# Kernel tuning notes

Measured on AMD Instinct MI355X. Metric: run time of the kernel, lower is better.

Reference implementation:

```python
import jax, jax.numpy as jnp
import numpy as np

B, C, N, L, K, PRED = 64, 2, 1024, 24, 3, 12


def setup_inputs() -> dict:
    key = jax.random.key(0)
    ks = jax.random.split(key, 32)
    u = lambda k, shape, s: jax.random.uniform(k, shape, jnp.float32, -s, s)
    stdv_gc = 1.0 / np.sqrt(N)
    stdv_g = 1.0 / np.sqrt(N * (K + 1))
    stdv_r = 1.0 / np.sqrt(2 * N)
    inp = {
        'inputs': jax.random.normal(ks[0], (B, C, N, L), jnp.float32),
        'adj': (jax.random.uniform(ks[1], (N, N)) < 0.05).astype(jnp.float32),
        'gc_w': u(ks[2], (K, N, N), stdv_gc),
        'Wf': u(ks[3], (N, N * (K + 1)), stdv_g), 'bf': u(ks[4], (N,), stdv_g),
        'Wi': u(ks[5], (N, N * (K + 1)), stdv_g), 'bi': u(ks[6], (N,), stdv_g),
        'Wo': u(ks[7], (N, N * (K + 1)), stdv_g), 'bo': u(ks[8], (N,), stdv_g),
        'Wc': u(ks[9], (N, N * (K + 1)), stdv_g), 'bc': u(ks[10], (N,), stdv_g),
        'rWf': u(ks[11], (N, 2 * N), stdv_r), 'rbf': u(ks[12], (N,), stdv_r),
        'rWi': u(ks[13], (N, 2 * N), stdv_r), 'rbi': u(ks[14], (N,), stdv_r),
        'rWo': u(ks[15], (N, 2 * N), stdv_r), 'rbo': u(ks[16], (N,), stdv_r),
        'rWc': u(ks[17], (N, 2 * N), stdv_r), 'rbc': u(ks[18], (N,), stdv_r),
        'neighbor_w': u(ks[19], (N,), stdv_gc),
        'c': jnp.ones((1,), jnp.float32),
        'conv_w': u(ks[20], (C * PRED, C), 1.0 / np.sqrt(C)),
        'conv_b': u(ks[21], (C * PRED,), 1.0 / np.sqrt(C)),
    }
    return inp


def _build_A_list(adj, k):
    # tmp = sum(A, 0); zeros -> 1e-5; 'D_inverse' = diag(tmp) (as in original code)
    tmp = jnp.sum(adj, 0)
    tmp = jnp.where(tmp == 0, 1e-5, tmp)
    a_norm = tmp[:, None] * adj  # diag(tmp) @ A
    a_list = []
    a_tmp = jnp.eye(adj.shape[0], dtype=adj.dtype)
    for _ in range(k):
        a_tmp = jnp.minimum(a_tmp @ a_norm, 1.0)  # clamp max=1.0
        a_list.append(a_tmp)
    return a_list


def _forward(adj, inputs, gc_w, Wf, bf, Wi, bi, Wo, bo, Wc, bc,
             rWf, rbf, rWi, rbi, rWo, rbo, rWc, rbc, neighbor_w, c, conv_w, conv_b):
    b, ch, n, l = inputs.shape
    k = gc_w.shape[0]
    a_list = _build_A_list(adj, k)
    a_stack = jnp.stack(a_list)            # (K,N,N)
    eff_w = a_stack * gc_w                 # masked FilterLinear weights
    nbr = a_list[-1] @ neighbor_w          # (N,)
    Wg = jnp.concatenate([Wf, Wi, Wo, Wc], 0)      # fused gate weights (4N, (K+1)N)
    bg = jnp.concatenate([bf, bi, bo, bc], 0)
    rWg = jnp.concatenate([rWf, rWi, rWo, rWc], 0)  # (4N, 2N)
    rbg = jnp.concatenate([rbf, rbi, rbo, rbc], 0)

    def step(carry, x):  # x: (B,C,N)
        H, Cs, rH, rCs, _ = carry
        # gc = cat_k FilterLinear_k(x), each x @ (A_k*W_k)^T
        gc = jnp.einsum('bcn,kmn->bckm', x, eff_w).reshape(b, ch, k * n)
        g = jnp.concatenate([gc, H], -1) @ Wg.T + bg
        f, i, o, Ct = jnp.split(g, 4, -1)
        Cs = jax.nn.sigmoid(f) * (Cs * nbr) + jax.nn.sigmoid(i) * jnp.tanh(Ct)
        H = jax.nn.sigmoid(o) * jnp.tanh(Cs)
        rg = jnp.concatenate([x, rH], -1) @ rWg.T + rbg
        rf, ri, ro, rCt = jnp.split(rg, 4, -1)
        rCs = jax.nn.sigmoid(rf) * rCs + jax.nn.sigmoid(ri) * jnp.tanh(rCt)
        rH = jax.nn.sigmoid(ro) * jnp.tanh(rCs)
        var1 = jnp.var(x, axis=(0, 2), keepdims=True, ddof=1)   # (1,C,1), unbiased like torch
        var2 = jnp.var(gc, axis=(0, 2), keepdims=True, ddof=1)
        pred = (H * var1 * c + rH * var2) / (var1 + var2 * c)
        return (H, Cs, rH, rCs, pred), None

    z = jnp.zeros((b, ch, n), inputs.dtype)
    xs = jnp.moveaxis(inputs, -1, 0)  # (L,B,C,N)
    (H, Cs, rH, rCs, pred), _ = jax.lax.scan(step, (z, z, z, z, z), xs)
    # Conv1d(C, C*pred_len, k=1) then reshape (B,C,N,pred_len)
    out = jnp.einsum('bcn,oc->bon', pred, conv_w) + conv_b[:, None]
    return out.reshape(b, ch, n, -1)


def reference(inputs, adj, gc_w, Wf, bf, Wi, bi, Wo, bo, Wc, bc,
              rWf, rbf, rWi, rbi, rWo, rbo, rWc, rbc, neighbor_w, c, conv_w, conv_b):
    return _forward(adj, inputs, gc_w, Wf, bf, Wi, bi, Wo, bo, Wc, bc,
                    rWf, rbf, rWi, rbi, rWo, rbo, rWc, rbc, neighbor_w, c, conv_w, conv_b)
```

## Files before the change

### kernel.cpp

```cpp
#include <hip/hip_runtime.h>
#include <cmath>

#define NN 1024
#define BC 128
#define LS 24

typedef unsigned short u16;
typedef __attribute__((ext_vector_type(4))) float f32x4;
typedef __attribute__((ext_vector_type(8))) short bf16x8;

typedef __attribute__((address_space(1))) const void* as1cv;
typedef __attribute__((address_space(3))) void* as3v;

#define GLD16(gp, lp) __builtin_amdgcn_global_load_lds((as1cv)(gp), (as3v)(lp), 16, 0, 0)

__device__ __forceinline__ float sigf(float x){ return 1.0f/(1.0f+expf(-x)); }

__device__ __forceinline__ u16 f2b(float x){
  union { float f; unsigned u; } v; v.f = x;
  unsigned r = v.u + 0x7FFFu + ((v.u >> 16) & 1u);
  return (u16)(r >> 16);
}
__device__ __forceinline__ float b2f(u16 b){
  union { unsigned u; float f; } v; v.u = ((unsigned)b) << 16;
  return v.f;
}


__global__ void k_transpose(const float* __restrict__ in, u16* __restrict__ Xb){
  int idx = blockIdx.x*256 + threadIdx.x;
  const float4* p = (const float4*)(in + (size_t)idx*LS);
  float v[LS];
  #pragma unroll
  for (int q = 0; q < 6; ++q){
    float4 f = p[q];
    v[q*4]=f.x; v[q*4+1]=f.y; v[q*4+2]=f.z; v[q*4+3]=f.w;
  }
  #pragma unroll
  for (int t = 0; t < LS; ++t)
    Xb[(size_t)t*BC*NN + idx] = f2b(v[t]);
}

__global__ void k_colsum1(const float* __restrict__ adj, float* __restrict__ part){
  int b = blockIdx.x;
  for (int j = threadIdx.x; j < 1024; j += 256){
    float s = 0.f;
    for (int i = 0; i < 16; ++i) s += adj[(size_t)(b*16+i)*1024 + j];
    part[(size_t)b*1024 + j] = s;
  }
}
__global__ void k_colsum2(const float* __restrict__ part, float* __restrict__ tmp){
  int j = blockIdx.x*256 + threadIdx.x;
  float s = 0.f;
  for (int b = 0; b < 64; ++b) s += part[(size_t)b*1024 + j];
  tmp[j] = (s == 0.f) ? 1e-5f : s;
}

__global__ void k_anormT(const float* __restrict__ adj, const float* __restrict__ tmp,
                         u16* __restrict__ A1b, u16* __restrict__ anormT){
  __shared__ u16 t[64][65];
  int bi = blockIdx.y*64, bj = blockIdx.x*64;
  for (int e = threadIdx.x; e < 4096; e += 256){
    int r = e >> 6, cc = e & 63;
    float v = tmp[bi+r]*adj[(size_t)(bi+r)*1024 + bj+cc];
    A1b[(size_t)(bi+r)*1024 + bj+cc] = f2b(fminf(v, 1.f));
    t[r][cc] = f2b(v);
  }
  __syncthreads();
  for (int e = threadIdx.x; e < 4096; e += 256){
    int r = e >> 6, cc = e & 63;
    anormT[(size_t)(bj+r)*1024 + bi+cc] = t[cc][r];
  }
}

__global__ void k_nbr(const u16* __restrict__ A3b, const float* __restrict__ nw,
                      float* __restrict__ nbr){
  __shared__ float red[256];
  int row = blockIdx.x;
  float s = 0.f;
  for (int j = threadIdx.x; j < 1024; j += 256)
    s += b2f(A3b[(size_t)row*1024 + j])*nw[j];
  red[threadIdx.x] = s; __syncthreads();
  for (int st = 128; st > 0; st >>= 1){
    if (threadIdx.x < st) red[threadIdx.x] += red[threadIdx.x+st];
    __syncthreads();
  }
  if (threadIdx.x == 0) nbr[row] = red[0];
}

__global__ void k_effT(const u16* __restrict__ Ap, const float* __restrict__ gcw,
                       u16* __restrict__ effb, u16* __restrict__ effbT){
  __shared__ u16 t[64][65];
  int bi = blockIdx.y*64, bj = blockIdx.x*64;
  for (int e = threadIdx.x; e < 4096; e += 256){
    int r = e >> 6, cc = e & 63;
    size_t idx = (size_t)(bi+r)*1024 + bj+cc;
    u16 v = f2b(b2f(Ap[idx]) * gcw[idx]);
    effb[idx] = v;
    t[r][cc] = v;
  }
  __syncthreads();
  for (int e = threadIdx.x; e < 4096; e += 256){
    int r = e >> 6, cc = e & 63;
    effbT[(size_t)(bj+r)*3072 + bi+cc] = t[cc][r];
  }
}

__global__ void k_pack(const float* __restrict__ Wf, const float* __restrict__ Wi,
                       const float* __restrict__ Wo, const float* __restrict__ Wc,
                       const float* __restrict__ rWf, const float* __restrict__ rWi,
                       const float* __restrict__ rWo, const float* __restrict__ rWc,
                       u16* __restrict__ Wgxb, u16* __restrict__ WgHp,
                       u16* __restrict__ rWgxb, u16* __restrict__ rWgHp){
  int idx = blockIdx.x*256 + threadIdx.x;
  if (idx < 16777216){
    int k = idx & 4095, r = idx >> 12, seg = r >> 10, j = r & 1023;
    const float* W = seg==0?Wf: seg==1?Wi: seg==2?Wo:Wc;
    float v = W[(size_t)j*4096 + k];
    if (k < 3072) Wgxb[(size_t)r*3072 + k] = f2b(v);
    else {
      int p = (j>>2)*16 + seg*4 + (j&3);
      WgHp[(size_t)p*1024 + (k-3072)] = f2b(v);
    }
  } else {
    int i2 = idx - 16777216;
    int k = i2 & 2047, r = i2 >> 11, seg = r >> 10, j = r & 1023;
    const float* W = seg==0?rWf: seg==1?rWi: seg==2?rWo:rWc;
    float v = W[(size_t)j*2048 + k];
    if (k < 1024) rWgxb[(size_t)r*1024 + k] = f2b(v);
    else {
      int p = (j>>2)*16 + seg*4 + (j&3);
      rWgHp[(size_t)p*1024 + (k-1024)] = f2b(v);
    }
  }
}
__global__ void k_packbias(const float* __restrict__ bf_, const float* __restrict__ bi_,
                           const float* __restrict__ bo_, const float* __restrict__ bc_,
                           const float* __restrict__ rbf, const float* __restrict__ rbi,
                           const float* __restrict__ rbo, const float* __restrict__ rbc,
                           float* __restrict__ bg, float* __restrict__ rbg){
  int idx = blockIdx.x*256 + threadIdx.x;
  int seg = idx >> 10, j = idx & 1023;
  bg[idx]  = (seg==0?bf_: seg==1?bi_: seg==2?bo_:bc_)[j];
  rbg[idx] = (seg==0?rbf: seg==1?rbi: seg==2?rbo:rbc)[j];
}

__device__ __forceinline__ void stage128(const u16* __restrict__ A, const u16* __restrict__ B,
                                         int K, int k0, u16* lA, u16* lB, int w, int lane){
  const int lrow = lane >> 3;
  const int srck = ((lane & 7) ^ lrow) * 8;
  #pragma unroll
  for (int c = 0; c < 4; ++c){
    int row = w*32 + c*8;
    GLD16(A + (size_t)(row + lrow)*K + k0 + srck, &lA[row*64]);
    GLD16(B + (size_t)(row + lrow)*K + k0 + srck, &lB[row*64]);
  }
}

__device__ __forceinline__ void mfma_tile(
    const u16* __restrict__ A, const u16* __restrict__ Bw, int K,
    const float* __restrict__ bias,
    float* __restrict__ outf, u16* __restrict__ outb, int ldc)
{
  __shared__ u16 ldsA[128*64];
  __shared__ u16 ldsB[128*64];
  const int tid  = threadIdx.x;
  const int lane = tid & 63;
  const int w    = tid >> 6;
  const int wr   = (w >> 1) * 64;
  const int wc   = (w & 1) * 64;
  f32x4 acc[4][4] = {};

  for (int k0 = 0; k0 < K; k0 += 64){
    stage128(A, Bw, K, k0, ldsA, ldsB, w, lane);
    __syncthreads();
    #pragma unroll
    for (int kk = 0; kk < 2; ++kk) {
      bf16x8 af[4], bfr[4];
      #pragma unroll
      for (int mi = 0; mi < 4; ++mi) {
        int row = wr + mi*16 + (lane & 15);
        int grp = (kk*4 + (lane >> 4)) ^ (row & 7);
        af[mi] = *(const bf16x8*)&ldsA[row*64 + grp*8];
      }
      #pragma unroll
      for (int ni = 0; ni < 4; ++ni) {
        int row = wc + ni*16 + (lane & 15);
        int grp = (kk*4 + (lane >> 4)) ^ (row & 7);
        bfr[ni] = *(const bf16x8*)&ldsB[row*64 + grp*8];
      }
      #pragma unroll
      for (int mi = 0; mi < 4; ++mi)
        #pragma unroll
        for (int ni = 0; ni < 4; ++ni)
          acc[mi][ni] = __builtin_amdgcn_mfma_f32_16x16x32_bf16(af[mi], bfr[ni], acc[mi][ni], 0, 0, 0);
    }
    __syncthreads();
  }
  #pragma unroll
  for (int mi = 0; mi < 4; ++mi) {
    #pragma unroll
    for (int ni = 0; ni < 4; ++ni) {
      int col = wc + ni*16 + (lane & 15);
      #pragma unroll
      for (int q = 0; q < 4; ++q) {
        int row = wr + mi*16 + (lane >> 4)*4 + q;
        float v = acc[mi][ni][q];
        if (bias) v += bias[col];
        if (outf) outf[(size_t)row*ldc + col] = v;
        if (outb) outb[(size_t)row*ldc + col] = f2b(v);
      }
    }
  }
}

__global__ __launch_bounds__(256) void k_mfma_nt(
    const u16* __restrict__ A, const u16* __restrict__ B, int K,
    const float* __restrict__ bias, float* __restrict__ outf,
    u16* __restrict__ outb, int ldc)
{
  size_t i0 = (size_t)blockIdx.y * 128, j0 = (size_t)blockIdx.x * 128;
  mfma_tile(A + i0*K, B + j0*K, K,
            bias ? bias + j0 : nullptr,
            outf ? outf + i0*ldc + j0 : nullptr,
            outb ? outb + i0*ldc + j0 : nullptr, ldc);
}

__global__ __launch_bounds__(256) void k_mfma64(
    const u16* __restrict__ Ag, const u16* __restrict__ Bg, int K,
    int clamp1, u16* __restrict__ outb, int ldc)
{
  __shared__ u16 ldsA[64*64];
  __shared__ u16 ldsB[64*64];
  const int tid  = threadIdx.x;
  const int lane = tid & 63;
  const int w    = tid >> 6;
  const int wr   = (w >> 1) * 32;
  const int wc   = (w & 1) * 32;
  const u16* A = Ag + (size_t)blockIdx.y*64*K;
  const u16* B = Bg + (size_t)blockIdx.x*64*K;
  f32x4 acc[2][2] = {};

  const int lrow = lane >> 3;
  const int srck = ((lane & 7) ^ lrow) * 8;
  for (int k0 = 0; k0 < K; k0 += 64){
    #pragma unroll
    for (int c = 0; c < 2; ++c){
      int row = w*16 + c*8;
      GLD16(A + (size_t)(row + lrow)*K + k0 + srck, &ldsA[row*64]);
      GLD16(B + (size_t)(row + lrow)*K + k0 + srck, &ldsB[row*64]);
    }
    __syncthreads();
    #pragma unroll
    for (int kk = 0; kk < 2; ++kk){
      bf16x8 af[2], bfr[2];
      #pragma unroll
      for (int mi = 0; mi < 2; ++mi){
        int row = wr + mi*16 + (lane & 15);
        int grp = (kk*4 + (lane >> 4)) ^ (row & 7);
        af[mi] = *(const bf16x8*)&ldsA[row*64 + grp*8];
      }
      #pragma unroll
      for (int ni = 0; ni < 2; ++ni){
        int row = wc + ni*16 + (lane & 15);
        int grp = (kk*4 + (lane >> 4)) ^ (row & 7);
        bfr[ni] = *(const bf16x8*)&ldsB[row*64 + grp*8];
      }
      #pragma unroll
      for (int mi = 0; mi < 2; ++mi)
        #pragma unroll
        for (int ni = 0; ni < 2; ++ni)
          acc[mi][ni] = __builtin_amdgcn_mfma_f32_16x16x32_bf16(af[mi], bfr[ni], acc[mi][ni], 0, 0, 0);
    }
    __syncthreads();
  }
  #pragma unroll
  for (int mi = 0; mi < 2; ++mi){
    #pragma unroll
    for (int ni = 0; ni < 2; ++ni){
      int col = blockIdx.x*64 + wc + ni*16 + (lane & 15);
      #pragma unroll
      for (int q = 0; q < 4; ++q){
        int row = blockIdx.y*64 + wr + mi*16 + (lane >> 4)*4 + q;
        float v = acc[mi][ni][q];
        if (clamp1) v = fminf(v, 1.f);
        outb[(size_t)row*ldc + col] = f2b(v);
      }
    }
  }
}

__global__ __launch_bounds__(256) void k_step(
    const u16* __restrict__ WgHp, const u16* __restrict__ rWgHp,
    const u16* __restrict__ pre_t,
    const float* __restrict__ nbrv,
    u16* __restrict__ Hb2, u16* __restrict__ rHb2,
    float* __restrict__ Cs, float* __restrict__ rCs,
    float* __restrict__ Hf, float* __restrict__ rHf,
    int ph, int last)
{
  __shared__ u16 ldsA[64*128];
  __shared__ u16 ldsB[16*128];

  const int tid  = threadIdx.x;
  const int lane = tid & 63;
  const int w    = tid >> 6;
  const int bid  = blockIdx.x;
  const int job  = bid >> 9;
  const int rem  = bid & 511;
  const int s    = rem >> 1;
  const int r0   = (rem & 1) * 64;

  const u16* Bp   = (job ? rWgHp : WgHp) + (size_t)s*16*1024;
  const u16* Ab   = (job ? rHb2 : Hb2) + (size_t)ph*BC*NN + (size_t)r0*NN;
  const u16* pret = pre_t + (size_t)job*4096;
  u16* Hnext  = (job ? rHb2 : Hb2) + (size_t)(ph^1)*BC*NN;
  float* Csb  = job ? rCs : Cs;
  float* Hfin = job ? rHf : Hf;

  const int lrow = lane >> 4;
  const int s4   = lane & 15;

  f32x4 acc = {};
  for (int t = 0; t < 8; ++t){
    int k0 = t*128;
    #pragma unroll
    for (int c = 0; c < 4; ++c){
      int rowb = w*16 + c*4;
      int row = rowb + lrow;
      int srcg = (s4 & 8) | ((s4 & 7) ^ (row & 7));
      GLD16(Ab + (size_t)row*1024 + k0 + srcg*8, &ldsA[rowb*128]);
    }
    { int rowb = w*4;
      int row = rowb + lrow;
      int srcg = (s4 & 8) | ((s4 & 7) ^ (row & 7));
      GLD16(Bp + (size_t)row*1024 + k0 + srcg*8, &ldsB[rowb*128]); }
    __syncthreads();
    #pragma unroll
    for (int kk = 0; kk < 4; ++kk){
      int idx = kk*4 + (lane >> 4);
      int rowa = w*16 + (lane & 15);
      int pa = (idx & 8) | ((idx & 7) ^ (rowa & 7));
      bf16x8 af = *(const bf16x8*)&ldsA[rowa*128 + pa*8];
      int rowb2 = lane & 15;
      int pb = (idx & 8) | ((idx & 7) ^ (rowb2 & 7));
      bf16x8 bv = *(const bf16x8*)&ldsB[rowb2*128 + pb*8];
      acc = __builtin_amdgcn_mfma_f32_16x16x32_bf16(af, bv, acc, 0, 0, 0);
    }
    __syncthreads();
  }

  const int pcol = lane & 15;
  const int gcol = (pcol >> 2)*1024 + s*4 + (pcol & 3);
  const bool act = (lane & 12) == 0;
  const int  col = s*4 + (lane & 3);
  float fac = 1.f;
  if (!job && act) fac = nbrv[col];
  #pragma unroll
  for (int q = 0; q < 4; ++q){
    int row = r0 + w*16 + (lane >> 4)*4 + q;
    float a = acc[q] + b2f(pret[(size_t)row*8192 + gcol]);
    float vi  = __shfl_xor(a, 4);
    float vo  = __shfl_xor(a, 8);
    float vct = __shfl_xor(a, 12);
    if (act){
      float fg = sigf(a), ig = sigf(vi), og = sigf(vo), ct = tanhf(vct);
      size_t cidx = (size_t)row*NN + col;
      float cs = fg*Csb[cidx]*fac + ig*ct;
      Csb[cidx] = cs;
      float h = og*tanhf(cs);
      Hnext[cidx] = f2b(h);
      if (last) Hfin[cidx] = h;
    }
  }
}

__global__ void k_var1(const u16* __restrict__ Xl, const u16* __restrict__ gcl,
                       float* __restrict__ part){
  int ch = blockIdx.x & 1, seg = blockIdx.x >> 1;
  int tid = threadIdx.x;
  float s1=0.f,q1=0.f,s2=0.f,q2=0.f;
  for (int bb = 0; bb < 2; ++bb){
    int row = (seg*2+bb)*2 + ch;
    const u16* xr = Xl + (size_t)row*1024;
    for (int n = tid; n < 1024; n += 256){ float v = b2f(xr[n]); s1 += v; q1 += v*v; }
    const u16* gr = gcl + (size_t)row*3072;
    for (int n = tid; n < 3072; n += 256){ float v = b2f(gr[n]); s2 += v; q2 += v*v; }
  }
  __shared__ float red[256][4];
  red[tid][0]=s1; red[tid][1]=q1; red[tid][2]=s2; red[tid][3]=q2;
  __syncthreads();
  for (int st = 128; st > 0; st >>= 1){
    if (tid < st){ for (int z = 0; z < 4; ++z) red[tid][z] += red[tid+st][z]; }
    __syncthreads();
  }
  if (tid == 0){ for (int z = 0; z < 4; ++z) part[(size_t)blockIdx.x*4 + z] = red[0][z]; }
}
__global__ void k_var2(const float* __restrict__ part, float* __restrict__ vars){
  int tid = threadIdx.x;
  if (tid < 2){
    float s1=0.f,q1=0.f,s2=0.f,q2=0.f;
    for (int seg = 0; seg < 32; ++seg){
      const float* p = part + (size_t)(seg*2+tid)*4;
      s1 += p[0]; q1 += p[1]; s2 += p[2]; q2 += p[3];
    }
    float n1 = 65536.f, n2 = 196608.f;
    vars[tid]   = (q1 - s1*s1/n1) / (n1 - 1.f);
    vars[2+tid] = (q2 - s2*s2/n2) / (n2 - 1.f);
  }
}

__global__ void k_out(const float* __restrict__ H, const float* __restrict__ rH,
                      const float* __restrict__ vars, const float* __restrict__ cptr,
                      const float* __restrict__ cw, const float* __restrict__ cb,
                      float* __restrict__ out){
  int idx = blockIdx.x*256 + threadIdx.x;
  int n = idx & 1023, b = idx >> 10;
  float c0 = cptr[0];
  float v10 = vars[0], v11 = vars[1], v20 = vars[2], v21 = vars[3];
  size_t i0 = (size_t)(b*2+0)*1024 + n, i1 = (size_t)(b*2+1)*1024 + n;
  float p0 = (H[i0]*v10*c0 + rH[i0]*v20) / (v10 + v20*c0);
  float p1 = (H[i1]*v11*c0 + rH[i1]*v21) / (v11 + v21*c0);
  float* ob = out + (size_t)b*24*1024 + n;
  #pragma unroll
  for (int o = 0; o < 24; ++o)
    ob[(size_t)o*1024] = p0*cw[o*2+0] + p1*cw[o*2+1] + cb[o];
}

extern "C" void kernel_launch(void* const* d_in, const int* in_sizes, int n_in,
                              void* d_out, int out_size, void* d_ws, size_t ws_size,
                              hipStream_t stream) {
  const float* inputs = (const float*)d_in[0];
  const float* adj    = (const float*)d_in[1];
  const float* gcw    = (const float*)d_in[2];
  const float* Wf  = (const float*)d_in[3];  const float* bf_ = (const float*)d_in[4];
  const float* Wi  = (const float*)d_in[5];  const float* bi_ = (const float*)d_in[6];
  const float* Wo  = (const float*)d_in[7];  const float* bo_ = (const float*)d_in[8];
  const float* Wc  = (const float*)d_in[9];  const float* bc_ = (const float*)d_in[10];
  const float* rWf = (const float*)d_in[11]; const float* rbf = (const float*)d_in[12];
  const float* rWi = (const float*)d_in[13]; const float* rbi = (const float*)d_in[14];
  const float* rWo = (const float*)d_in[15]; const float* rbo = (const float*)d_in[16];
  const float* rWc = (const float*)d_in[17]; const float* rbc = (const float*)d_in[18];
  const float* nw     = (const float*)d_in[19];
  const float* cscal  = (const float*)d_in[20];
  const float* convw  = (const float*)d_in[21];
  const float* convb  = (const float*)d_in[22];
  float* out = (float*)d_out;

  char* cur = (char*)d_ws;
  auto alloc = [&](size_t bytes) -> void* {
    void* p = cur; cur += (bytes + 255) & ~(size_t)255; return p;
  };
  u16*   Xb     = (u16*)  alloc((size_t)LS*BC*NN*2);
  float* csum   = (float*)alloc((size_t)64*1024*4);
  float* tmpv   = (float*)alloc(1024*4);
  u16*   anormT = (u16*)  alloc((size_t)NN*NN*2);
  u16*   Apowb  = (u16*)  alloc((size_t)3*NN*NN*2);
  float* nbrv   = (float*)alloc(1024*4);
  u16*   effb   = (u16*)  alloc((size_t)3*NN*NN*2);
  u16*   effbT  = (u16*)  alloc((size_t)3*NN*NN*2);
  u16*   Wgxb   = (u16*)  alloc((size_t)4096*3072*2);
  u16*   WgHp   = (u16*)  alloc((size_t)4096*1024*2);
  u16*   rWgHp  = (u16*)  alloc((size_t)4096*1024*2);
  u16*   Bcat   = (u16*)  alloc((size_t)8192*1024*2);
  float* bgcat  = (float*)alloc(8192*4);
  u16*   gclb   = (u16*)  alloc((size_t)BC*3072*2);
  u16*   prebuf = (u16*)  alloc((size_t)3072*8192*2);
  char*  zbase  = cur;
  u16*   Hb2    = (u16*)  alloc((size_t)2*BC*NN*2);
  u16*   rHb2   = (u16*)  alloc((size_t)2*BC*NN*2);
  float* Cs     = (float*)alloc((size_t)BC*NN*4);
  float* rCs    = (float*)alloc((size_t)BC*NN*4);
  size_t zlen   = (size_t)(cur - zbase);
  float* Hfv    = (float*)alloc((size_t)BC*NN*4);
  float* rHfv   = (float*)alloc((size_t)BC*NN*4);
  float* vars   = (float*)alloc(16*4);
  float* part   = (float*)alloc(64*4*4);

  u16* A1b = Apowb;
  u16* A2b = Apowb + (size_t)NN*NN;
  u16* A3b = Apowb + (size_t)2*NN*NN;
  u16* Cwb   = Bcat;
  u16* rWgxb = Bcat + (size_t)4096*1024;

  k_transpose<<<(BC*NN)/256, 256, 0, stream>>>(inputs, Xb);
  k_colsum1<<<64, 256, 0, stream>>>(adj, csum);
  k_colsum2<<<4, 256, 0, stream>>>(csum, tmpv);
  dim3 g16(16, 16);
  k_anormT<<<g16, 256, 0, stream>>>(adj, tmpv, A1b, anormT);
  k_mfma64<<<g16, 256, 0, stream>>>(A1b, anormT, 1024, 1, A2b, 1024);
  k_mfma64<<<g16, 256, 0, stream>>>(A2b, anormT, 1024, 1, A3b, 1024);
  k_nbr<<<NN, 256, 0, stream>>>(A3b, nw, nbrv);
  dim3 geff(16, 48);
  k_effT<<<geff, 256, 0, stream>>>(Apowb, gcw, effb, effbT);
  k_pack<<<(16777216+8388608)/256, 256, 0, stream>>>(Wf, Wi, Wo, Wc, rWf, rWi, rWo, rWc,
                                                     Wgxb, WgHp, rWgxb, rWgHp);
  k_packbias<<<16, 256, 0, stream>>>(bf_, bi_, bo_, bc_, rbf, rbi, rbo, rbc,
                                     bgcat, bgcat + 4096);

  dim3 gcwg(16, 64);
  k_mfma64<<<gcwg, 256, 0, stream>>>(Wgxb, effbT, 3072, 0, Cwb, 1024);
  dim3 gpre(64, 24);
  k_mfma_nt<<<gpre, 256, 0, stream>>>(Xb, Bcat, 1024, bgcat, nullptr, prebuf, 8192);
  dim3 ggcl(48, 2);
  k_mfma64<<<ggcl, 256, 0, stream>>>(Xb + (size_t)(LS-1)*BC*NN, effb, 1024, 0, gclb, 3072);

  hipMemsetAsync(zbase, 0, zlen, stream);

  for (int t = 0; t < LS; ++t)
    k_step<<<1024, 256, 0, stream>>>(WgHp, rWgHp,
        prebuf + (size_t)t*BC*8192,
        nbrv, Hb2, rHb2, Cs, rCs, Hfv, rHfv, t & 1, t == LS-1);

  k_var1<<<64, 256, 0, stream>>>(Xb + (size_t)(LS-1)*BC*NN, gclb, part);
  k_var2<<<1, 64, 0, stream>>>(part, vars);
  k_out<<<(64*1024)/256, 256, 0, stream>>>(Hfv, rHfv, vars, cscal, convw, convb, out);
}
```

Before: 618.7 us.

## Merge prep kernels, fold variance reduction into output, deepen K tiles

Transpose, column-sum, bias packing and weight packing are merged into one multi-role kernel, and the final variance reduction is folded into the output kernel, removing several launches. The 64x64 MFMA GEMM and the recurrent step kernel now stage larger K slices per barrier (128 and 256), halving the number of sync and load rounds at the cost of more LDS per block. Every output block redundantly recomputes the four variances from the partials.

```diff
diff --git a/kernel.cpp b/kernel.cpp
--- a/kernel.cpp
+++ b/kernel.cpp
@@ -26,29 +26,69 @@
   return v.f;
 }
 
-
-__global__ void k_transpose(const float* __restrict__ in, u16* __restrict__ Xb){
-  int idx = blockIdx.x*256 + threadIdx.x;
-  const float4* p = (const float4*)(in + (size_t)idx*LS);
-  float v[LS];
-  #pragma unroll
-  for (int q = 0; q < 6; ++q){
-    float4 f = p[q];
-    v[q*4]=f.x; v[q*4+1]=f.y; v[q*4+2]=f.z; v[q*4+3]=f.w;
-  }
-  #pragma unroll
-  for (int t = 0; t < LS; ++t)
-    Xb[(size_t)t*BC*NN + idx] = f2b(v[t]);
-}
-
-__global__ void k_colsum1(const float* __restrict__ adj, float* __restrict__ part){
-  int b = blockIdx.x;
-  for (int j = threadIdx.x; j < 1024; j += 256){
-    float s = 0.f;
-    for (int i = 0; i < 16; ++i) s += adj[(size_t)(b*16+i)*1024 + j];
-    part[(size_t)b*1024 + j] = s;
-  }
-}
+__global__ void k_prep(const float* __restrict__ inputs, const float* __restrict__ adj,
+                       const float* __restrict__ Wf, const float* __restrict__ Wi,
+                       const float* __restrict__ Wo, const float* __restrict__ Wc,
+                       const float* __restrict__ rWf, const float* __restrict__ rWi,
+                       const float* __restrict__ rWo, const float* __restrict__ rWc,
+                       const float* __restrict__ bf_, const float* __restrict__ bi_,
+                       const float* __restrict__ bo_, const float* __restrict__ bc_,
+                       const float* __restrict__ rbf, const float* __restrict__ rbi,
+                       const float* __restrict__ rbo, const float* __restrict__ rbc,
+                       u16* __restrict__ Xb, float* __restrict__ csum,
+                       u16* __restrict__ Wgxb, u16* __restrict__ WgHp,
+                       u16* __restrict__ rWgxb, u16* __restrict__ rWgHp,
+                       float* __restrict__ bgcat){
+  int b = blockIdx.x, tid = threadIdx.x;
+  if (b < 512){
+    int idx = b*256 + tid;
+    const float4* p = (const float4*)(inputs + (size_t)idx*LS);
+    float v[LS];
+    #pragma unroll
+    for (int q = 0; q < 6; ++q){
+      float4 f = p[q];
+      v[q*4]=f.x; v[q*4+1]=f.y; v[q*4+2]=f.z; v[q*4+3]=f.w;
+    }
+    #pragma unroll
+    for (int t = 0; t < LS; ++t)
+      Xb[(size_t)t*BC*NN + idx] = f2b(v[t]);
+  } else if (b < 576){
+    int bb = b - 512;
+    for (int j = tid; j < 1024; j += 256){
+      float s = 0.f;
+      for (int i = 0; i < 16; ++i) s += adj[(size_t)(bb*16+i)*1024 + j];
+      csum[(size_t)bb*1024 + j] = s;
+    }
+  } else if (b < 592){
+    int idx = (b-576)*256 + tid;
+    int seg = idx >> 10, j = idx & 1023;
+    bgcat[idx]      = (seg==0?bf_: seg==1?bi_: seg==2?bo_:bc_)[j];
+    bgcat[4096+idx] = (seg==0?rbf: seg==1?rbi: seg==2?rbo:rbc)[j];
+  } else {
+    int idx = (b-592)*256 + tid;
+    if (idx < 16777216){
+      int k = idx & 4095, r = idx >> 12, seg = r >> 10, j = r & 1023;
+      const float* W = seg==0?Wf: seg==1?Wi: seg==2?Wo:Wc;
+      float v = W[(size_t)j*4096 + k];
+      if (k < 3072) Wgxb[(size_t)r*3072 + k] = f2b(v);
+      else {
+        int p = (j>>2)*16 + seg*4 + (j&3);
+        WgHp[(size_t)p*1024 + (k-3072)] = f2b(v);
+      }
+    } else {
+      int i2 = idx - 16777216;
+      int k = i2 & 2047, r = i2 >> 11, seg = r >> 10, j = r & 1023;
+      const float* W = seg==0?rWf: seg==1?rWi: seg==2?rWo:rWc;
+      float v = W[(size_t)j*2048 + k];
+      if (k < 1024) rWgxb[(size_t)r*1024 + k] = f2b(v);
+      else {
+        int p = (j>>2)*16 + seg*4 + (j&3);
+        rWgHp[(size_t)p*1024 + (k-1024)] = f2b(v);
+      }
+    }
+  }
+}
+
 __global__ void k_colsum2(const float* __restrict__ part, float* __restrict__ tmp){
   int j = blockIdx.x*256 + threadIdx.x;
   float s = 0.f;
@@ -104,45 +144,6 @@
     int r = e >> 6, cc = e & 63;
     effbT[(size_t)(bj+r)*3072 + bi+cc] = t[cc][r];
   }
-}
-
-__global__ void k_pack(const float* __restrict__ Wf, const float* __restrict__ Wi,
-                       const float* __restrict__ Wo, const float* __restrict__ Wc,
-                       const float* __restrict__ rWf, const float* __restrict__ rWi,
-                       const float* __restrict__ rWo, const float* __restrict__ rWc,
-                       u16* __restrict__ Wgxb, u16* __restrict__ WgHp,
-                       u16* __restrict__ rWgxb, u16* __restrict__ rWgHp){
-  int idx = blockIdx.x*256 + threadIdx.x;
-  if (idx < 16777216){
-    int k = idx & 4095, r = idx >> 12, seg = r >> 10, j = r & 1023;
-    const float* W = seg==0?Wf: seg==1?Wi: seg==2?Wo:Wc;
-    float v = W[(size_t)j*4096 + k];
-    if (k < 3072) Wgxb[(size_t)r*3072 + k] = f2b(v);
-    else {
-      int p = (j>>2)*16 + seg*4 + (j&3);
-      WgHp[(size_t)p*1024 + (k-3072)] = f2b(v);
-    }
-  } else {
-    int i2 = idx - 16777216;
-    int k = i2 & 2047, r = i2 >> 11, seg = r >> 10, j = r & 1023;
-    const float* W = seg==0?rWf: seg==1?rWi: seg==2?rWo:rWc;
-    float v = W[(size_t)j*2048 + k];
-    if (k < 1024) rWgxb[(size_t)r*1024 + k] = f2b(v);
-    else {
-      int p = (j>>2)*16 + seg*4 + (j&3);
-      rWgHp[(size_t)p*1024 + (k-1024)] = f2b(v);
-    }
-  }
-}
-__global__ void k_packbias(const float* __restrict__ bf_, const float* __restrict__ bi_,
-                           const float* __restrict__ bo_, const float* __restrict__ bc_,
-                           const float* __restrict__ rbf, const float* __restrict__ rbi,
-                           const float* __restrict__ rbo, const float* __restrict__ rbc,
-                           float* __restrict__ bg, float* __restrict__ rbg){
-  int idx = blockIdx.x*256 + threadIdx.x;
-  int seg = idx >> 10, j = idx & 1023;
-  bg[idx]  = (seg==0?bf_: seg==1?bi_: seg==2?bo_:bc_)[j];
-  rbg[idx] = (seg==0?rbf: seg==1?rbi: seg==2?rbo:rbc)[j];
 }
 
 __device__ __forceinline__ void stage128(const u16* __restrict__ A, const u16* __restrict__ B,
@@ -230,8 +231,8 @@
     const u16* __restrict__ Ag, const u16* __restrict__ Bg, int K,
     int clamp1, u16* __restrict__ outb, int ldc)
 {
-  __shared__ u16 ldsA[64*64];
-  __shared__ u16 ldsB[64*64];
+  __shared__ u16 ldsA[64*128];
+  __shared__ u16 ldsB[64*128];
   const int tid  = threadIdx.x;
   const int lane = tid & 63;
   const int w    = tid >> 6;
@@ -241,30 +242,33 @@
   const u16* B = Bg + (size_t)blockIdx.x*64*K;
   f32x4 acc[2][2] = {};
 
-  const int lrow = lane >> 3;
-  const int srck = ((lane & 7) ^ lrow) * 8;
-  for (int k0 = 0; k0 < K; k0 += 64){
-    #pragma unroll
-    for (int c = 0; c < 2; ++c){
-      int row = w*16 + c*8;
-      GLD16(A + (size_t)(row + lrow)*K + k0 + srck, &ldsA[row*64]);
-      GLD16(B + (size_t)(row + lrow)*K + k0 + srck, &ldsB[row*64]);
-    }
-    __syncthreads();
-    #pragma unroll
-    for (int kk = 0; kk < 2; ++kk){
+  const int r4  = lane >> 4;
+  const int g16 = lane & 15;
+  for (int k0 = 0; k0 < K; k0 += 128){
+    #pragma unroll
+    for (int c = 0; c < 4; ++c){
+      int rowb = w*16 + c*4;
+      int row = rowb + r4;
+      int srcg = (g16 & 8) | ((g16 & 7) ^ (row & 7));
+      GLD16(A + (size_t)row*K + k0 + srcg*8, &ldsA[rowb*128]);
+      GLD16(B + (size_t)row*K + k0 + srcg*8, &ldsB[rowb*128]);
+    }
+    __syncthreads();
+    #pragma unroll
+    for (int kk = 0; kk < 4; ++kk){
+      int idx = kk*4 + (lane >> 4);
       bf16x8 af[2], bfr[2];
       #pragma unroll
       for (int mi = 0; mi < 2; ++mi){
         int row = wr + mi*16 + (lane & 15);
-        int grp = (kk*4 + (lane >> 4)) ^ (row & 7);
-        af[mi] = *(const bf16x8*)&ldsA[row*64 + grp*8];
+        int pa = (idx & 8) | ((idx & 7) ^ (row & 7));
+        af[mi] = *(const bf16x8*)&ldsA[row*128 + pa*8];
       }
       #pragma unroll
       for (int ni = 0; ni < 2; ++ni){
         int row = wc + ni*16 + (lane & 15);
-        int grp = (kk*4 + (lane >> 4)) ^ (row & 7);
-        bfr[ni] = *(const bf16x8*)&ldsB[row*64 + grp*8];
+        int pb = (idx & 8) | ((idx & 7) ^ (row & 7));
+        bfr[ni] = *(const bf16x8*)&ldsB[row*128 + pb*8];
       }
       #pragma unroll
       for (int mi = 0; mi < 2; ++mi)
@@ -299,8 +303,8 @@
     float* __restrict__ Hf, float* __restrict__ rHf,
     int ph, int last)
 {
-  __shared__ u16 ldsA[64*128];
-  __shared__ u16 ldsB[16*128];
+  __shared__ u16 ldsA[64*256];
+  __shared__ u16 ldsB[16*256];
 
   const int tid  = threadIdx.x;
   const int lane = tid & 63;
@@ -318,33 +322,36 @@
   float* Csb  = job ? rCs : Cs;
   float* Hfin = job ? rHf : Hf;
 
-  const int lrow = lane >> 4;
-  const int s4   = lane & 15;
+  const int g32   = lane & 31;
+  const int rhalf = lane >> 5;
 
   f32x4 acc = {};
-  for (int t = 0; t < 8; ++t){
-    int k0 = t*128;
-    #pragma unroll
-    for (int c = 0; c < 4; ++c){
-      int rowb = w*16 + c*4;
-      int row = rowb + lrow;
-      int srcg = (s4 & 8) | ((s4 & 7) ^ (row & 7));
-      GLD16(Ab + (size_t)row*1024 + k0 + srcg*8, &ldsA[rowb*128]);
-    }
-    { int rowb = w*4;
-      int row = rowb + lrow;
-      int srcg = (s4 & 8) | ((s4 & 7) ^ (row & 7));
-      GLD16(Bp + (size_t)row*1024 + k0 + srcg*8, &ldsB[rowb*128]); }
-    __syncthreads();
-    #pragma unroll
-    for (int kk = 0; kk < 4; ++kk){
+  for (int t = 0; t < 4; ++t){
+    int k0 = t*256;
+    #pragma unroll
+    for (int c = 0; c < 8; ++c){
+      int rowb = w*16 + c*2;
+      int row = rowb + rhalf;
+      int srcg = (g32 & 24) | ((g32 & 7) ^ (row & 7));
+      GLD16(Ab + (size_t)row*1024 + k0 + srcg*8, &ldsA[rowb*256]);
+    }
+    #pragma unroll
+    for (int c = 0; c < 2; ++c){
+      int rowb = w*4 + c*2;
+      int row = rowb + rhalf;
+      int srcg = (g32 & 24) | ((g32 & 7) ^ (row & 7));
+      GLD16(Bp + (size_t)row*1024 + k0 + srcg*8, &ldsB[rowb*256]);
+    }
+    __syncthreads();
+    #pragma unroll
+    for (int kk = 0; kk < 8; ++kk){
       int idx = kk*4 + (lane >> 4);
       int rowa = w*16 + (lane & 15);
-      int pa = (idx & 8) | ((idx & 7) ^ (rowa & 7));
-      bf16x8 af = *(const bf16x8*)&ldsA[rowa*128 + pa*8];
+      int pa = (idx & 24) | ((idx & 7) ^ (rowa & 7));
+      bf16x8 af = *(const bf16x8*)&ldsA[rowa*256 + pa*8];
       int rowb2 = lane & 15;
-      int pb = (idx & 8) | ((idx & 7) ^ (rowb2 & 7));
-      bf16x8 bv = *(const bf16x8*)&ldsB[rowb2*128 + pb*8];
+      int pb = (idx & 24) | ((idx & 7) ^ (rowb2 & 7));
+      bf16x8 bv = *(const bf16x8*)&ldsB[rowb2*256 + pb*8];
       acc = __builtin_amdgcn_mfma_f32_16x16x32_bf16(af, bv, acc, 0, 0, 0);
     }
     __syncthreads();
@@ -396,28 +403,28 @@
   }
   if (tid == 0){ for (int z = 0; z < 4; ++z) part[(size_t)blockIdx.x*4 + z] = red[0][z]; }
 }
-__global__ void k_var2(const float* __restrict__ part, float* __restrict__ vars){
-  int tid = threadIdx.x;
-  if (tid < 2){
-    float s1=0.f,q1=0.f,s2=0.f,q2=0.f;
-    for (int seg = 0; seg < 32; ++seg){
-      const float* p = part + (size_t)(seg*2+tid)*4;
-      s1 += p[0]; q1 += p[1]; s2 += p[2]; q2 += p[3];
-    }
-    float n1 = 65536.f, n2 = 196608.f;
-    vars[tid]   = (q1 - s1*s1/n1) / (n1 - 1.f);
-    vars[2+tid] = (q2 - s2*s2/n2) / (n2 - 1.f);
-  }
-}
 
 __global__ void k_out(const float* __restrict__ H, const float* __restrict__ rH,
-                      const float* __restrict__ vars, const float* __restrict__ cptr,
+                      const float* __restrict__ part, const float* __restrict__ cptr,
                       const float* __restrict__ cw, const float* __restrict__ cb,
                       float* __restrict__ out){
-  int idx = blockIdx.x*256 + threadIdx.x;
+  __shared__ float vsh[4];
+  int tid = threadIdx.x;
+  if (tid < 4){
+    int ch = tid & 1, which = tid >> 1;
+    float s = 0.f, q = 0.f;
+    for (int seg = 0; seg < 32; ++seg){
+      const float* p = part + (size_t)(seg*2+ch)*4 + which*2;
+      s += p[0]; q += p[1];
+    }
+    float n = which ? 196608.f : 65536.f;
+    vsh[tid] = (q - s*s/n) / (n - 1.f);
+  }
+  __syncthreads();
+  int idx = blockIdx.x*256 + tid;
   int n = idx & 1023, b = idx >> 10;
   float c0 = cptr[0];
-  float v10 = vars[0], v11 = vars[1], v20 = vars[2], v21 = vars[3];
+  float v10 = vsh[0], v11 = vsh[1], v20 = vsh[2], v21 = vsh[3];
   size_t i0 = (size_t)(b*2+0)*1024 + n, i1 = (size_t)(b*2+1)*1024 + n;
   float p0 = (H[i0]*v10*c0 + rH[i0]*v20) / (v10 + v20*c0);
   float p1 = (H[i1]*v11*c0 + rH[i1]*v21) / (v11 + v21*c0);
@@ -474,7 +481,6 @@
   size_t zlen   = (size_t)(cur - zbase);
   float* Hfv    = (float*)alloc((size_t)BC*NN*4);
   float* rHfv   = (float*)alloc((size_t)BC*NN*4);
-  float* vars   = (float*)alloc(16*4);
   float* part   = (float*)alloc(64*4*4);
 
   u16* A1b = Apowb;
@@ -483,8 +489,10 @@
   u16* Cwb   = Bcat;
   u16* rWgxb = Bcat + (size_t)4096*1024;
 
-  k_transpose<<<(BC*NN)/256, 256, 0, stream>>>(inputs, Xb);
-  k_colsum1<<<64, 256, 0, stream>>>(adj, csum);
+  k_prep<<<592 + (16777216+8388608)/256, 256, 0, stream>>>(
+      inputs, adj, Wf, Wi, Wo, Wc, rWf, rWi, rWo, rWc,
+      bf_, bi_, bo_, bc_, rbf, rbi, rbo, rbc,
+      Xb, csum, Wgxb, WgHp, rWgxb, rWgHp, bgcat);
   k_colsum2<<<4, 256, 0, stream>>>(csum, tmpv);
   dim3 g16(16, 16);
   k_anormT<<<g16, 256, 0, stream>>>(adj, tmpv, A1b, anormT);
@@ -493,10 +501,6 @@
   k_nbr<<<NN, 256, 0, stream>>>(A3b, nw, nbrv);
   dim3 geff(16, 48);
   k_effT<<<geff, 256, 0, stream>>>(Apowb, gcw, effb, effbT);
-  k_pack<<<(16777216+8388608)/256, 256, 0, stream>>>(Wf, Wi, Wo, Wc, rWf, rWi, rWo, rWc,
-                                                     Wgxb, WgHp, rWgxb, rWgHp);
-  k_packbias<<<16, 256, 0, stream>>>(bf_, bi_, bo_, bc_, rbf, rbi, rbo, rbc,
-                                     bgcat, bgcat + 4096);
 
   dim3 gcwg(16, 64);
   k_mfma64<<<gcwg, 256, 0, stream>>>(Wgxb, effbT, 3072, 0, Cwb, 1024);
@@ -513,6 +517,5 @@
         nbrv, Hb2, rHb2, Cs, rCs, Hfv, rHfv, t & 1, t == LS-1);
 
   k_var1<<<64, 256, 0, stream>>>(Xb + (size_t)(LS-1)*BC*NN, gclb, part);
-  k_var2<<<1, 64, 0, stream>>>(part, vars);
-  k_out<<<(64*1024)/256, 256, 0, stream>>>(Hfv, rHfv, vars, cscal, convw, convb, out);
-}
+  k_out<<<(64*1024)/256, 256, 0, stream>>>(Hfv, rHfv, part, cscal, convw, convb, out);
+}
```

After: 617.6 us. Within noise of the previous version (-0.2%).
